# Performance work log

Measured on AMD Instinct MI355X. Metric: run time of the kernel, lower is better.

The kernel has to match this reference:

```python
import jax, jax.numpy as jnp
import numpy as np

MC = 16384
IND_T = 96
N_MAT = 4
N_STRIKES = 21


def _init_linear(key, fan_in, fan_out, prefix=()):
    k1, k2 = jax.random.split(key)
    lim = 1.0 / np.sqrt(fan_in)
    W = jax.random.uniform(k1, prefix + (fan_in, fan_out), minval=-lim, maxval=lim, dtype=jnp.float32)
    b = jax.random.uniform(k2, prefix + (fan_out,), minval=-lim, maxval=lim, dtype=jnp.float32)
    return W, b


def setup_inputs() -> dict:
    key = jax.random.key(0)
    ks = jax.random.split(key, 14)
    z = jax.random.normal(ks[0], (MC, IND_T), dtype=jnp.float32)
    zz = jax.random.normal(ks[1], (MC, IND_T), dtype=jnp.float32)
    timegrid = jnp.arange(IND_T + 1, dtype=jnp.float32) / 365.0  # daily grid
    maturities = jnp.array([24, 48, 72, 96], dtype=jnp.int32)    # in days
    strikes = jnp.linspace(0.8, 1.2, N_STRIKES, dtype=jnp.float32)
    sv_W1, sv_b1 = _init_linear(ks[2], 3, 100)
    sv_W2, sv_b2 = _init_linear(ks[3], 100, 100)
    sv_W3, sv_b3 = _init_linear(ks[4], 100, 1)
    vh_W1, vh_b1 = _init_linear(ks[5], 2, 20, (N_MAT,))
    vh_W2, vh_b2 = _init_linear(ks[6], 20, N_STRIKES, (N_MAT,))
    vd_W1, vd_b1 = _init_linear(ks[7], 1, 20)
    vd_W2, vd_b2 = _init_linear(ks[8], 20, 1)
    vv_W1, vv_b1 = _init_linear(ks[9], 1, 20)
    vv_W2, vv_b2 = _init_linear(ks[10], 20, 1)
    v0 = jax.random.uniform(ks[11], (1,), dtype=jnp.float32) * 0.1
    rho = jnp.ones((1,), dtype=jnp.float32) * -2.0
    return dict(S0=jnp.float32(1.0), rate=jnp.float32(0.05), z=z, zz=zz,
                timegrid=timegrid, strikes=strikes, v0=v0, rho=rho,
                sv_W1=sv_W1, sv_b1=sv_b1, sv_W2=sv_W2, sv_b2=sv_b2, sv_W3=sv_W3, sv_b3=sv_b3,
                vh_W1=vh_W1, vh_b1=vh_b1, vh_W2=vh_W2, vh_b2=vh_b2,
                vd_W1=vd_W1, vd_b1=vd_b1, vd_W2=vd_W2, vd_b2=vd_b2,
                vv_W1=vv_W1, vv_b1=vv_b1, vv_W2=vv_W2, vv_b2=vv_b2,
                maturities=maturities)


def reference(S0, rate, z, zz, timegrid, strikes, v0, rho,
              sv_W1, sv_b1, sv_W2, sv_b2, sv_W3, sv_b3,
              vh_W1, vh_b1, vh_W2, vh_b2,
              vd_W1, vd_b1, vd_W2, vd_b2,
              vv_W1, vv_b1, vv_W2, vv_b2,
              maturities):
    sg = jax.lax.stop_gradient
    mc = z.shape[0]
    n_mat = vh_W1.shape[0]
    n_strikes = strikes.shape[0]

    def s_vol(x):  # [MC,3] -> [MC,1], softplus output
        h1 = jax.nn.relu(x @ sv_W1 + sv_b1)
        h2 = jax.nn.relu(h1 @ sv_W2 + sv_b2)
        return jax.nn.softplus(h2 @ sv_W3 + sv_b3)

    def v_drift(v):  # [MC,1] -> [MC,1]
        return jax.nn.relu(v @ vd_W1 + vd_b1) @ vd_W2 + vd_b2

    def v_vol(v):  # [MC,1] -> [MC,1], softplus output
        return jax.nn.softplus(jax.nn.relu(v @ vv_W1 + vv_b1) @ vv_W2 + vv_b2)

    def vanilla_hedge_all(x):  # [MC,2] -> [MC, n_strikes, n_mat] (one net per maturity)
        h1 = jax.nn.relu(jnp.einsum('mi,kio->kmo', x, vh_W1) + vh_b1[:, None, :])
        out = jax.nn.softplus(jnp.einsum('kmo,koj->kmj', h1, vh_W2) + vh_b2[:, None, :])
        return jnp.transpose(out, (1, 2, 0))

    rho_t = jnp.tanh(rho)[0]
    days = jnp.round(timegrid * 365.0).astype(jnp.int32)       # [IND_T+1]
    le = days[1:, None] <= maturities[None, :]                  # [IND_T, n_mat]
    idx_net = jnp.argmax(le, axis=1)                            # first live maturity per step
    is_mat = jnp.any(days[1:, None] == maturities[None, :], axis=1)
    mat_idx = jnp.arange(n_mat)

    Slog0 = jnp.log(jnp.full((mc, 1), S0, dtype=jnp.float32))
    V0 = jnp.full((mc, 1), 1.0, dtype=jnp.float32) * jax.nn.sigmoid(v0)[0] * 0.5
    cv0 = jnp.zeros((mc, n_strikes, n_mat), dtype=jnp.float32)
    pv0 = jnp.zeros((n_mat, n_strikes), dtype=jnp.float32)

    xs = (z.T[:, :, None], zz.T[:, :, None], timegrid[:-1], timegrid[1:], idx_net, is_mat)

    def step(carry, x):
        Slog_old, V_old, cv, pv_h, pv_var = carry
        z_i, zz_i, t0, t1, idx, im = x
        h = t1 - t0
        sqh = jnp.sqrt(h)
        dW = sqh * z_i                                          # [MC,1]
        dB = rho_t * dW + jnp.sqrt(1.0 - rho_t ** 2) * sqh * zz_i
        ones_t = jnp.full((mc, 1), 1.0, dtype=jnp.float32) * t0
        pd = s_vol(jnp.concatenate([ones_t, Slog_old, V_old], axis=1))  # price diffusion
        cv_fwd = vanilla_hedge_all(jnp.concatenate([ones_t, sg(Slog_old)], axis=1))
        V_new = V_old + v_drift(V_old) * h + v_vol(V_old) * dB
        drift = rate - 0.5 * pd ** 2
        diff = pd * dW
        drift_c = 1.0 + jnp.abs(sg(drift)) * sqh                # tamed Euler
        diff_c = 1.0 + jnp.abs(sg(pd)) * sqh
        Slog_new = Slog_old + drift * h / drift_c + diff / diff_c
        S_new = jnp.exp(Slog_new)
        S_old = jnp.exp(Slog_old)
        dS = jnp.exp(-rate * t1) * S_new - jnp.exp(-rate * t0) * S_old  # [MC,1]
        mask = (mat_idx >= idx).astype(cv.dtype)                # live maturities only
        cv = cv + mask[None, None, :] * cv_fwd * sg(dS)[:, :, None]
        # hedged vanilla (call) prices collected at maturity steps
        payoff = jnp.exp(-rate * t1) * jnp.maximum(S_new - strikes[None, :], 0.0)
        price = payoff - cv[:, :, idx]                          # [MC, n_strikes]
        pv = jnp.mean(price, axis=0)
        pvar = jnp.var(price, axis=0, ddof=1)
        sel = (mat_idx == idx)[:, None] & im
        pv_h = jnp.where(sel, pv[None, :], pv_h)
        pv_var = jnp.where(sel, pvar[None, :], pv_var)
        return (Slog_new, V_new, cv, pv_h, pv_var), None

    (_, _, _, pv_h, pv_var), _ = jax.lax.scan(step, (Slog0, V0, cv0, pv0, pv0), xs)
    return jnp.stack([pv_h, pv_var])  # [2, n_mat, n_strikes]
```

## Files before the change

kernel.cpp:

```cpp
#include <hip/hip_runtime.h>
#include <hip/hip_bf16.h>
#include <math.h>


#define MC      16384
#define NSTEP   96
#define BLOCK   512
#define NGROUP  512
#define NPAIR   84

typedef short bf16x8 __attribute__((ext_vector_type(8)));
typedef float f32x4  __attribute__((ext_vector_type(4)));

union U8 { uint4 u; bf16x8 v; };
union BF2U { __hip_bfloat162 b; unsigned u; };

__device__ __forceinline__ unsigned bf16rne(float x) {
    unsigned u = __float_as_uint(x);
    return (u + 0x7FFFu + ((u >> 16) & 1u)) >> 16;
}
__device__ __forceinline__ unsigned pk2(float lo, float hi) {
    BF2U t; t.b = __float22bfloat162_rn(make_float2(lo, hi));
    return t.u;
}
__device__ __forceinline__ float sp(float x) {
    return fmaxf(x, 0.f) + __logf(1.f + __expf(-fabsf(x)));
}

__global__ __launch_bounds__(BLOCK, 4)
void lsv_sim(const float* __restrict__ S0p,   const float* __restrict__ ratep,
             const float* __restrict__ z,     const float* __restrict__ zzg,
             const float* __restrict__ strikesg,
             const float* __restrict__ v0p,   const float* __restrict__ rhop,
             const float* __restrict__ svW1,  const float* __restrict__ svb1,
             const float* __restrict__ svW2,  const float* __restrict__ svb2,
             const float* __restrict__ svW3,  const float* __restrict__ svb3,
             const float* __restrict__ vhW1,  const float* __restrict__ vhb1,
             const float* __restrict__ vhW2,  const float* __restrict__ vhb2,
             const float* __restrict__ vdW1,  const float* __restrict__ vdb1,
             const float* __restrict__ vdW2,  const float* __restrict__ vdb2,
             const float* __restrict__ vvW1,  const float* __restrict__ vvb1,
             const float* __restrict__ vvW2,  const float* __restrict__ vvb2,
             const int*   __restrict__ mats,
             float* __restrict__ psum, float* __restrict__ psq)
{
    __shared__ __align__(16) unsigned short H1c[16 * 32 * 8];
    __shared__ __align__(16) float W1f[16 * 32];
    __shared__ __align__(16) float WH1f[16 * 32];
    __shared__ __align__(16) float B2T[128], W3T[128];
    __shared__ __align__(16) float RED[32 * 4];
    __shared__ float VDb[2][32], VVb[2][32];
    __shared__ float PSs[2][32], PSq[2][32];
    __shared__ __align__(16) float VW[128];
    __shared__ __align__(16) float4 STEP[NSTEP];
    __shared__ float D1T[NSTEP];
    __shared__ int   ITAB[NSTEP];
    __shared__ float ZT[32][97], ZZT[32][97];
    __shared__ float SLOG[32], VST[32], SST[32], SLOGP[32], DSP[32];
    __shared__ __align__(16) float CW1[2][128];
    __shared__ __align__(16) float CH[2][128];

    const int tid  = threadIdx.x;
    const int lane = tid & 63;
    const int w    = __builtin_amdgcn_readfirstlane(tid >> 6);
    const int quad = lane >> 4;
    const int col  = lane & 15;
    const int lp   = lane & 31;

    const int pt = w & 1;
    const int jg = w >> 1;
    const int hm = w >> 1;
    const int path = pt * 16 + col;
    const int kc   = jg * 4 + quad;

    {
        const size_t gbase = (size_t)blockIdx.x * 32 * NSTEP;
        for (int e = tid; e < 32 * NSTEP; e += BLOCK) {
            const int p = e / NSTEP, ii = e - p * NSTEP;
            ZT[p][ii]  = z  [gbase + e];
            ZZT[p][ii] = zzg[gbase + e];
        }
    }
    for (int e = tid; e < 128; e += BLOCK) {
        float v = 0.f;
        if      (e < 20)             v = vdW1[e];
        else if (e < 40)             v = vdb1[e - 20];
        else if (e < 60)             v = vdW2[e - 40];
        else if (e >= 64 && e < 84)  v = vvW1[e - 64];
        else if (e >= 84 && e < 104) v = vvb1[e - 84];
        else if (e >= 104 && e < 124)v = vvW2[e - 104];
        else if (e == 124)           v = vdb2[0];
        else if (e == 125)           v = vvb2[0];
        VW[e] = v;
        B2T[e] = (e < 100) ? svb2[e] : 0.f;
        W3T[e] = (e < 100) ? svW3[e] : 0.f;
    }
    for (int e = tid; e < 512; e += BLOCK) {
        const int kc2 = e >> 5, r5 = e & 31, grp = r5 >> 3, kk = kc2 * 8 + (r5 & 7);
        float v = 0.f;
        if (kk < 100) v = (grp == 0) ? svW1[kk] : (grp == 1) ? svW1[100 + kk]
                        : (grp == 2) ? svW1[200 + kk] : svb1[kk];
        W1f[e] = v;
    }
    for (int e = tid; e < 512; e += BLOCK) {
        const int hq = e >> 5, r5 = e & 31, grp = r5 >> 3;
        const int hmm = hq >> 2, qq = hq & 3;
        const int j = qq * 8 + (r5 & 7);
        float v = 0.f;
        if (j < 20 && grp < 3)
            v = (grp == 0) ? vhW1[hmm * 40 + j] : (grp == 1) ? vhW1[hmm * 40 + 20 + j]
                                                : vhb1[hmm * 20 + j];
        WH1f[e] = v;
    }

    const float rate  = ratep[0];
    const float S0    = S0p[0];
    const float rho_t = tanhf(rhop[0]);
    const float srho  = sqrtf(1.f - rho_t * rho_t);
    const float b3    = svb3[0];

    if (tid < NSTEP) {
        const int i = tid;
        const float t0 = (float)i       * (1.f / 365.f);
        const float t1 = (float)(i + 1) * (1.f / 365.f);
        const float h  = t1 - t0;
        STEP[i] = make_float4(t0, h, sqrtf(h), __expf(-rate * t0));
        D1T[i]  = __expf(-rate * t1);
        const int day = i + 1;
        const int m0 = mats[0], m1 = mats[1], m2 = mats[2], m3 = mats[3];
        const int idx = (day > m0) + (day > m1) + (day > m2);
        const int mi  = (idx == 0) ? m0 : (idx == 1) ? m1 : (idx == 2) ? m2 : m3;
        ITAB[i] = idx | ((day == mi) ? 256 : 0);
    }

    bf16x8 Af[4][2];
#pragma unroll
    for (int c = 0; c < 4; c++)
#pragma unroll
        for (int t = 0; t < 2; t++) {
            U8 tt;
#pragma unroll
            for (int e2 = 0; e2 < 4; e2++) {
                const int k0 = 32 * c + 8 * quad + 2 * e2;
                const int j  = (2 * jg + t) * 16 + col;
                const float v0 = (k0     < 100 && j < 100) ? svW2[k0 * 100 + j]       : 0.f;
                const float v1 = (k0 + 1 < 100 && j < 100) ? svW2[(k0 + 1) * 100 + j] : 0.f;
                (&tt.u.x)[e2] = bf16rne(v0) | (bf16rne(v1) << 16);
            }
            Af[c][t] = tt.v;
        }
    bf16x8 Ah[2];
#pragma unroll
    for (int st = 0; st < 2; st++) {
        U8 tt;
#pragma unroll
        for (int e2 = 0; e2 < 4; e2++) {
            const int j0 = 8 * quad + 2 * e2, j1 = j0 + 1;
            const int s  = (st == 0) ? col : (16 + (col & 3) * 4 + (col >> 2));
            const float v0 = (j0 < 20 && s < 21) ? vhW2[hm * 420 + j0 * 21 + s] : 0.f;
            const float v1 = (j1 < 20 && s < 21) ? vhW2[hm * 420 + j1 * 21 + s] : 0.f;
            (&tt.u.x)[e2] = bf16rne(v0) | (bf16rne(v1) << 16);
        }
        Ah[st] = tt.v;
    }
    f32x4 c0h, c1h;
    float K0a[4], K1a[2];
#pragma unroll
    for (int r = 0; r < 4; r++) {
        const int s0 = quad * 4 + r;
        c0h[r] = vhb2[hm * 21 + s0];
        K0a[r] = strikesg[s0];
        const int s1 = 16 + r * 4 + quad;
        c1h[r] = (s1 < 21) ? vhb2[hm * 21 + s1] : 0.f;
        if (r < 2) K1a[r] = (s1 < 21) ? strikesg[s1] : 1e30f;
    }

    float Slog = __logf(S0);
    float S    = __expf(Slog);
    float V    = (1.f / (1.f + __expf(-v0p[0]))) * 0.5f;
    f32x4 cv0 = {0.f, 0.f, 0.f, 0.f};
    float cv1[2] = {0.f, 0.f};

    __syncthreads();

    if (tid < 128) {
        const float t00 = STEP[0].x;
        const int kk = tid;
        CW1[0][kk] = fmaf(t00, W1f[(kk >> 3) * 32 + (kk & 7)],
                               W1f[(kk >> 3) * 32 + 24 + (kk & 7)]);
    } else if (tid < 256) {
        const float t00 = STEP[0].x;
        const int e = tid - 128;
        CH[0][e] = fmaf(t00, WH1f[(e >> 3) * 32 + (e & 7)],
                             WH1f[(e >> 3) * 32 + 16 + (e & 7)]);
    }
    if (tid < 32) {
        SLOG[tid] = Slog;
        SST[tid]  = S;
        VST[tid]  = V;
    }

    __syncthreads();

    const int j0e = (2 * jg) * 16 + quad * 4;
    const float4 b2a = *reinterpret_cast<const float4*>(B2T + j0e);
    const float4 w3a = *reinterpret_cast<const float4*>(W3T + j0e);
    const float4 b2b = *reinterpret_cast<const float4*>(B2T + j0e + 16);
    const float4 w3b = *reinterpret_cast<const float4*>(W3T + j0e + 16);
    const float4 wsA = *reinterpret_cast<const float4*>(WH1f + kc * 32 + 8);
    const float4 wsB = *reinterpret_cast<const float4*>(WH1f + kc * 32 + 12);
    const float4 w1B0 = *reinterpret_cast<const float4*>(W1f + kc * 32 + 8);
    const float4 w1B1 = *reinterpret_cast<const float4*>(W1f + kc * 32 + 12);
    const float4 w1C0 = *reinterpret_cast<const float4*>(W1f + kc * 32 + 16);
    const float4 w1C1 = *reinterpret_cast<const float4*>(W1f + kc * 32 + 20);

    auto hedge_step = [&](int ip) {
        const int iv   = ITAB[ip];
        const int idxp = iv & 0xff;
        if (hm >= idxp) {
            const int hb = ip & 1;
            const float slp = SLOGP[path];
            U8 b;
            {
                const float4 ch4 = *reinterpret_cast<const float4*>(&CH[hb][kc * 8]);
                (&b.u.x)[0] = pk2(fmaxf(ch4.x + slp * wsA.x, 0.f),
                                  fmaxf(ch4.y + slp * wsA.y, 0.f));
                (&b.u.x)[1] = pk2(fmaxf(ch4.z + slp * wsA.z, 0.f),
                                  fmaxf(ch4.w + slp * wsA.w, 0.f));
            }
            {
                const float4 ch4 = *reinterpret_cast<const float4*>(&CH[hb][kc * 8 + 4]);
                (&b.u.x)[2] = pk2(fmaxf(ch4.x + slp * wsB.x, 0.f),
                                  fmaxf(ch4.y + slp * wsB.y, 0.f));
                (&b.u.x)[3] = pk2(fmaxf(ch4.z + slp * wsB.z, 0.f),
                                  fmaxf(ch4.w + slp * wsB.w, 0.f));
            }
            const f32x4 D0 = __builtin_amdgcn_mfma_f32_16x16x32_bf16(Ah[0], b.v, c0h, 0, 0, 0);
            const f32x4 D1 = __builtin_amdgcn_mfma_f32_16x16x32_bf16(Ah[1], b.v, c1h, 0, 0, 0);
            const float dsP = DSP[path];
#pragma unroll
            for (int r = 0; r < 4; r++)
                cv0[r] += sp(D0[r]) * dsP;
#pragma unroll
            for (int r = 0; r < 2; r++)
                cv1[r] += sp(D1[r]) * dsP;
            if ((iv & 256) && hm == idxp) {
                const float Sp  = SST[path];
                const float d1p = D1T[ip];
                float p0[4], q0[4], p1[2], q1[2];
#pragma unroll
                for (int r = 0; r < 4; r++) {
                    p0[r] = d1p * fmaxf(Sp - K0a[r], 0.f) - cv0[r];
                    q0[r] = p0[r] * p0[r];
                }
#pragma unroll
                for (int r = 0; r < 2; r++) {
                    p1[r] = d1p * fmaxf(Sp - K1a[r], 0.f) - cv1[r];
                    q1[r] = p1[r] * p1[r];
                }
#pragma unroll
                for (int o = 1; o <= 8; o <<= 1) {
#pragma unroll
                    for (int r = 0; r < 4; r++) {
                        p0[r] += __shfl_xor(p0[r], o);
                        q0[r] += __shfl_xor(q0[r], o);
                    }
#pragma unroll
                    for (int r = 0; r < 2; r++) {
                        p1[r] += __shfl_xor(p1[r], o);
                        q1[r] += __shfl_xor(q1[r], o);
                    }
                }
                if (col == 0) {
#pragma unroll
                    for (int r = 0; r < 4; r++) {
                        const int s0 = quad * 4 + r;
                        PSs[pt][s0] = p0[r];  PSq[pt][s0] = q0[r];
                    }
#pragma unroll
                    for (int r = 0; r < 2; r++) {
                        const int s1 = 16 + r * 4 + quad;
                        if (s1 < 21) { PSs[pt][s1] = p1[r];  PSq[pt][s1] = q1[r]; }
                    }
                }
            }
        }
    };

    auto ps_reduce = [&](int ip) {
        if (w == 0) {
            const int iv = ITAB[ip];
            if (iv & 256) {
                const int s = lane & 31;
                if (s < 21) {
                    const float* src = (lane >= 32) ? &PSq[0][0] : &PSs[0][0];
                    const float acc = src[s] + src[32 + s];
                    float* dst = (lane >= 32) ? psq : psum;
                    dst[((iv & 0xff) * 21 + s) * NGROUP + blockIdx.x] = acc;
                }
            }
        }
    };

    for (int i = 0; i < NSTEP; i++) {
        const int buf = i & 1;

        {
            const float slp = SLOG[path];
            const float vp  = VST[path];
            uint4 o;
            {
                const float4 cw = *reinterpret_cast<const float4*>(&CW1[buf][kc * 8]);
                const float x0 = fmaxf(cw.x + slp * w1B0.x + vp * w1C0.x, 0.f);
                const float x1 = fmaxf(cw.y + slp * w1B0.y + vp * w1C0.y, 0.f);
                const float x2 = fmaxf(cw.z + slp * w1B0.z + vp * w1C0.z, 0.f);
                const float x3 = fmaxf(cw.w + slp * w1B0.w + vp * w1C0.w, 0.f);
                o.x = pk2(x0, x1);
                o.y = pk2(x2, x3);
            }
            {
                const float4 cw = *reinterpret_cast<const float4*>(&CW1[buf][kc * 8 + 4]);
                const float x0 = fmaxf(cw.x + slp * w1B1.x + vp * w1C1.x, 0.f);
                const float x1 = fmaxf(cw.y + slp * w1B1.y + vp * w1C1.y, 0.f);
                const float x2 = fmaxf(cw.z + slp * w1B1.z + vp * w1C1.z, 0.f);
                const float x3 = fmaxf(cw.w + slp * w1B1.w + vp * w1C1.w, 0.f);
                o.z = pk2(x0, x1);
                o.w = pk2(x2, x3);
            }
            *reinterpret_cast<uint4*>(H1c + (kc * 32 + path) * 8) = o;
        }
        if (i > 0) hedge_step(i - 1);
        if (w == 0) {
            const float Vp = VST[lp];
            const float* bw = VW + ((lane >= 32) ? 64 : 0);
            float a2 = 0.f;
#pragma unroll
            for (int q5 = 0; q5 < 5; q5++) {
                const float4 w1 = *reinterpret_cast<const float4*>(bw + 4 * q5);
                const float4 b1 = *reinterpret_cast<const float4*>(bw + 20 + 4 * q5);
                const float4 w2 = *reinterpret_cast<const float4*>(bw + 40 + 4 * q5);
                a2 += fmaxf(Vp * w1.x + b1.x, 0.f) * w2.x;
                a2 += fmaxf(Vp * w1.y + b1.y, 0.f) * w2.y;
                a2 += fmaxf(Vp * w1.z + b1.z, 0.f) * w2.z;
                a2 += fmaxf(Vp * w1.w + b1.w, 0.f) * w2.w;
            }
            if (lane < 32) VDb[buf][lp] = a2; else VVb[buf][lp] = a2;
        }
        __syncthreads();

        {
            f32x4 d0 = {0.f, 0.f, 0.f, 0.f};
            f32x4 d1 = {0.f, 0.f, 0.f, 0.f};
#pragma unroll
            for (int c = 0; c < 4; c++) {
                const bf16x8 b = *reinterpret_cast<const bf16x8*>(
                    H1c + ((quad + 4 * c) * 32 + path) * 8);
                d0 = __builtin_amdgcn_mfma_f32_16x16x32_bf16(Af[c][0], b, d0, 0, 0, 0);
                d1 = __builtin_amdgcn_mfma_f32_16x16x32_bf16(Af[c][1], b, d1, 0, 0, 0);
            }
            float acc = fmaxf(d0[0] + b2a.x, 0.f) * w3a.x
                      + fmaxf(d0[1] + b2a.y, 0.f) * w3a.y
                      + fmaxf(d0[2] + b2a.z, 0.f) * w3a.z
                      + fmaxf(d0[3] + b2a.w, 0.f) * w3a.w
                      + fmaxf(d1[0] + b2b.x, 0.f) * w3b.x
                      + fmaxf(d1[1] + b2b.y, 0.f) * w3b.y
                      + fmaxf(d1[2] + b2b.z, 0.f) * w3b.z
                      + fmaxf(d1[3] + b2b.w, 0.f) * w3b.w;
            acc += __shfl_xor(acc, 16);
            acc += __shfl_xor(acc, 32);
            if (quad == 0)
                RED[path * 4 + jg] = acc;
        }
        if (i > 0) ps_reduce(i - 1);
        __syncthreads();

        if (w == 1) {
            const float4 rr = *reinterpret_cast<const float4*>(RED + lp * 4);
            const float pout = (rr.x + rr.y) + (rr.z + rr.w);
            const float pd = sp(pout + b3);
            const float vdv = VDb[buf][lp] + VW[124];
            const float vvv = sp(VVb[buf][lp] + VW[125]);
            const float4 u  = STEP[i];
            const float sqh = u.z;
            const float zi  = ZT[lp][i];
            const float zzi = ZZT[lp][i];
            const float dW = sqh * zi;
            const float dB = rho_t * dW + srho * sqh * zzi;
            const float Vold = VST[lp];
            const float Sold = SST[lp];
            const float SlogO = SLOG[lp];
            const float Vn = Vold + vdv * u.y + vvv * dB;
            const float drift   = rate - 0.5f * pd * pd;
            const float diff    = pd * dW;
            const float drift_c = 1.f + fabsf(drift) * sqh;
            const float diff_c  = 1.f + fabsf(pd) * sqh;
            const float Sln = SlogO + __fdividef(drift * u.y, drift_c) + __fdividef(diff, diff_c);
            const float Sn  = __expf(Sln);
            const float dS  = D1T[i] * Sn - u.w * Sold;
            if (lane < 32) {
                SLOGP[lp] = SlogO;  DSP[lp] = dS;
                SLOG[lp]  = Sln;    SST[lp] = Sn;  VST[lp] = Vn;
            }
        } else if ((w == 2 || w == 3) && i + 1 < NSTEP) {
            const float t0n = STEP[i + 1].x;
            const int kk = (w - 2) * 64 + lane;
            CW1[buf ^ 1][kk] = fmaf(t0n, W1f[(kk >> 3) * 32 + (kk & 7)],
                                         W1f[(kk >> 3) * 32 + 24 + (kk & 7)]);
        } else if ((w == 4 || w == 5) && i + 1 < NSTEP) {
            const float t0n = STEP[i + 1].x;
            const int e = (w - 4) * 64 + lane;
            CH[buf ^ 1][e] = fmaf(t0n, WH1f[(e >> 3) * 32 + (e & 7)],
                                       WH1f[(e >> 3) * 32 + 16 + (e & 7)]);
        }
        __syncthreads();
    }

    hedge_step(NSTEP - 1);
    __syncthreads();
    ps_reduce(NSTEP - 1);
}

__global__ void lsv_finalize(const float* __restrict__ psum,
                             const float* __restrict__ psq,
                             float* __restrict__ out)
{
    const int t    = blockIdx.x;
    const int lane = threadIdx.x;
    float s = 0.f, q = 0.f;
    for (int b = lane; b < NGROUP; b += 64) {
        s += psum[t * NGROUP + b];
        q += psq [t * NGROUP + b];
    }
#pragma unroll
    for (int o = 1; o <= 32; o <<= 1) {
        s += __shfl_xor(s, o);
        q += __shfl_xor(q, o);
    }
    if (lane == 0) {
        const float mean = s * (1.0f / (float)MC);
        const float var  = (q - (float)MC * mean * mean) * (1.0f / (float)(MC - 1));
        out[t]         = mean;
        out[NPAIR + t] = var;
    }
}

extern "C" void kernel_launch(void* const* d_in, const int* in_sizes, int n_in,
                              void* d_out, int out_size, void* d_ws, size_t ws_size,
                              hipStream_t stream)
{
    const float* S0    = (const float*)d_in[0];
    const float* rate  = (const float*)d_in[1];
    const float* z     = (const float*)d_in[2];
    const float* zz    = (const float*)d_in[3];
    const float* strikes = (const float*)d_in[5];
    const float* v0    = (const float*)d_in[6];
    const float* rho   = (const float*)d_in[7];
    const float* svW1  = (const float*)d_in[8];
    const float* svb1  = (const float*)d_in[9];
    const float* svW2  = (const float*)d_in[10];
    const float* svb2  = (const float*)d_in[11];
    const float* svW3  = (const float*)d_in[12];
    const float* svb3  = (const float*)d_in[13];
    const float* vhW1  = (const float*)d_in[14];
    const float* vhb1  = (const float*)d_in[15];
    const float* vhW2  = (const float*)d_in[16];
    const float* vhb2  = (const float*)d_in[17];
    const float* vdW1  = (const float*)d_in[18];
    const float* vdb1  = (const float*)d_in[19];
    const float* vdW2  = (const float*)d_in[20];
    const float* vdb2  = (const float*)d_in[21];
    const float* vvW1  = (const float*)d_in[22];
    const float* vvb1  = (const float*)d_in[23];
    const float* vvW2  = (const float*)d_in[24];
    const float* vvb2  = (const float*)d_in[25];
    const int*   mats  = (const int*)d_in[26];

    float* psum = (float*)d_ws;
    float* psq  = psum + NPAIR * NGROUP;

    hipLaunchKernelGGL(lsv_sim, dim3(NGROUP), dim3(BLOCK), 0, stream,
                       S0, rate, z, zz, strikes, v0, rho,
                       svW1, svb1, svW2, svb2, svW3, svb3,
                       vhW1, vhb1, vhW2, vhb2,
                       vdW1, vdb1, vdW2, vdb2,
                       vvW1, vvb1, vvW2, vvb2,
                       mats, psum, psq);

    hipLaunchKernelGGL(lsv_finalize, dim3(NPAIR), dim3(64), 0, stream,
                       psum, psq, (float*)d_out);
}
```

Baseline: 440.9 us.

## Move loop-invariant weights from registers to LDS to raise occupancy

Raises the launch bound's minimum blocks per SM from 4 to 6. Hedge biases, strikes and first-layer weight slices that were held in registers for the whole loop are now staged in shared memory and reloaded inside each step where they are used. The aim is to lower VGPR pressure so more waves fit per CU and latency is hidden better. The cost is extra LDS reads every step, and spilling if the compiler cannot meet the tighter register budget.

```diff
diff --git a/kernel.cpp b/kernel.cpp
--- a/kernel.cpp
+++ b/kernel.cpp
@@ -27,7 +27,7 @@
     return fmaxf(x, 0.f) + __logf(1.f + __expf(-fabsf(x)));
 }
 
-__global__ __launch_bounds__(BLOCK, 4)
+__global__ __launch_bounds__(BLOCK, 6)
 void lsv_sim(const float* __restrict__ S0p,   const float* __restrict__ ratep,
              const float* __restrict__ z,     const float* __restrict__ zzg,
              const float* __restrict__ strikesg,
@@ -48,6 +48,8 @@
     __shared__ __align__(16) float W1f[16 * 32];
     __shared__ __align__(16) float WH1f[16 * 32];
     __shared__ __align__(16) float B2T[128], W3T[128];
+    __shared__ __align__(16) float BH0[64], BH1[64];
+    __shared__ __align__(16) float SK0[16], SK1[16];
     __shared__ __align__(16) float RED[32 * 4];
     __shared__ float VDb[2][32], VVb[2][32];
     __shared__ float PSs[2][32], PSq[2][32];
@@ -95,6 +97,16 @@
         B2T[e] = (e < 100) ? svb2[e] : 0.f;
         W3T[e] = (e < 100) ? svW3[e] : 0.f;
     }
+    for (int e = tid; e < 64; e += BLOCK) {
+        const int hmm = e >> 4, q = (e >> 2) & 3, r = e & 3;
+        BH0[e] = vhb2[hmm * 21 + q * 4 + r];
+        const int s1 = 16 + r * 4 + q;
+        BH1[e] = (s1 < 21) ? vhb2[hmm * 21 + s1] : 0.f;
+    }
+    if (tid < 16) {
+        SK0[tid] = strikesg[tid];
+        SK1[tid] = (16 + tid < 21) ? strikesg[16 + tid] : 1e30f;
+    }
     for (int e = tid; e < 512; e += BLOCK) {
         const int kc2 = e >> 5, r5 = e & 31, grp = r5 >> 3, kk = kc2 * 8 + (r5 & 7);
         float v = 0.f;
@@ -163,17 +175,6 @@
         }
         Ah[st] = tt.v;
     }
-    f32x4 c0h, c1h;
-    float K0a[4], K1a[2];
-#pragma unroll
-    for (int r = 0; r < 4; r++) {
-        const int s0 = quad * 4 + r;
-        c0h[r] = vhb2[hm * 21 + s0];
-        K0a[r] = strikesg[s0];
-        const int s1 = 16 + r * 4 + quad;
-        c1h[r] = (s1 < 21) ? vhb2[hm * 21 + s1] : 0.f;
-        if (r < 2) K1a[r] = (s1 < 21) ? strikesg[s1] : 1e30f;
-    }
 
     float Slog = __logf(S0);
     float S    = __expf(Slog);
@@ -203,16 +204,6 @@
     __syncthreads();
 
     const int j0e = (2 * jg) * 16 + quad * 4;
-    const float4 b2a = *reinterpret_cast<const float4*>(B2T + j0e);
-    const float4 w3a = *reinterpret_cast<const float4*>(W3T + j0e);
-    const float4 b2b = *reinterpret_cast<const float4*>(B2T + j0e + 16);
-    const float4 w3b = *reinterpret_cast<const float4*>(W3T + j0e + 16);
-    const float4 wsA = *reinterpret_cast<const float4*>(WH1f + kc * 32 + 8);
-    const float4 wsB = *reinterpret_cast<const float4*>(WH1f + kc * 32 + 12);
-    const float4 w1B0 = *reinterpret_cast<const float4*>(W1f + kc * 32 + 8);
-    const float4 w1B1 = *reinterpret_cast<const float4*>(W1f + kc * 32 + 12);
-    const float4 w1C0 = *reinterpret_cast<const float4*>(W1f + kc * 32 + 16);
-    const float4 w1C1 = *reinterpret_cast<const float4*>(W1f + kc * 32 + 20);
 
     auto hedge_step = [&](int ip) {
         const int iv   = ITAB[ip];
@@ -220,23 +211,30 @@
         if (hm >= idxp) {
             const int hb = ip & 1;
             const float slp = SLOGP[path];
+            const float* Wp = WH1f + (hm * 4 + quad) * 32;
+            const float4 wsA = *reinterpret_cast<const float4*>(Wp + 8);
+            const float4 wsB = *reinterpret_cast<const float4*>(Wp + 12);
             U8 b;
             {
-                const float4 ch4 = *reinterpret_cast<const float4*>(&CH[hb][kc * 8]);
+                const float4 ch4 = *reinterpret_cast<const float4*>(&CH[hb][(hm * 4 + quad) * 8]);
                 (&b.u.x)[0] = pk2(fmaxf(ch4.x + slp * wsA.x, 0.f),
                                   fmaxf(ch4.y + slp * wsA.y, 0.f));
                 (&b.u.x)[1] = pk2(fmaxf(ch4.z + slp * wsA.z, 0.f),
                                   fmaxf(ch4.w + slp * wsA.w, 0.f));
             }
             {
-                const float4 ch4 = *reinterpret_cast<const float4*>(&CH[hb][kc * 8 + 4]);
+                const float4 ch4 = *reinterpret_cast<const float4*>(&CH[hb][(hm * 4 + quad) * 8 + 4]);
                 (&b.u.x)[2] = pk2(fmaxf(ch4.x + slp * wsB.x, 0.f),
                                   fmaxf(ch4.y + slp * wsB.y, 0.f));
                 (&b.u.x)[3] = pk2(fmaxf(ch4.z + slp * wsB.z, 0.f),
                                   fmaxf(ch4.w + slp * wsB.w, 0.f));
             }
-            const f32x4 D0 = __builtin_amdgcn_mfma_f32_16x16x32_bf16(Ah[0], b.v, c0h, 0, 0, 0);
-            const f32x4 D1 = __builtin_amdgcn_mfma_f32_16x16x32_bf16(Ah[1], b.v, c1h, 0, 0, 0);
+            const float4 bh0 = *reinterpret_cast<const float4*>(BH0 + hm * 16 + quad * 4);
+            const float4 bh1 = *reinterpret_cast<const float4*>(BH1 + hm * 16 + quad * 4);
+            const f32x4 c0 = {bh0.x, bh0.y, bh0.z, bh0.w};
+            const f32x4 c1 = {bh1.x, bh1.y, bh1.z, bh1.w};
+            const f32x4 D0 = __builtin_amdgcn_mfma_f32_16x16x32_bf16(Ah[0], b.v, c0, 0, 0, 0);
+            const f32x4 D1 = __builtin_amdgcn_mfma_f32_16x16x32_bf16(Ah[1], b.v, c1, 0, 0, 0);
             const float dsP = DSP[path];
 #pragma unroll
             for (int r = 0; r < 4; r++)
@@ -247,15 +245,18 @@
             if ((iv & 256) && hm == idxp) {
                 const float Sp  = SST[path];
                 const float d1p = D1T[ip];
+                const float4 k0 = *reinterpret_cast<const float4*>(SK0 + quad * 4);
                 float p0[4], q0[4], p1[2], q1[2];
-#pragma unroll
-                for (int r = 0; r < 4; r++) {
-                    p0[r] = d1p * fmaxf(Sp - K0a[r], 0.f) - cv0[r];
-                    q0[r] = p0[r] * p0[r];
-                }
+                p0[0] = d1p * fmaxf(Sp - k0.x, 0.f) - cv0[0];
+                p0[1] = d1p * fmaxf(Sp - k0.y, 0.f) - cv0[1];
+                p0[2] = d1p * fmaxf(Sp - k0.z, 0.f) - cv0[2];
+                p0[3] = d1p * fmaxf(Sp - k0.w, 0.f) - cv0[3];
+#pragma unroll
+                for (int r = 0; r < 4; r++) q0[r] = p0[r] * p0[r];
 #pragma unroll
                 for (int r = 0; r < 2; r++) {
-                    p1[r] = d1p * fmaxf(Sp - K1a[r], 0.f) - cv1[r];
+                    const float K = SK1[r * 4 + quad];
+                    p1[r] = d1p * fmaxf(Sp - K, 0.f) - cv1[r];
                     q1[r] = p1[r] * p1[r];
                 }
 #pragma unroll
@@ -308,24 +309,19 @@
         {
             const float slp = SLOG[path];
             const float vp  = VST[path];
+            const float* Wp = W1f + kc * 32;
             uint4 o;
-            {
-                const float4 cw = *reinterpret_cast<const float4*>(&CW1[buf][kc * 8]);
-                const float x0 = fmaxf(cw.x + slp * w1B0.x + vp * w1C0.x, 0.f);
-                const float x1 = fmaxf(cw.y + slp * w1B0.y + vp * w1C0.y, 0.f);
-                const float x2 = fmaxf(cw.z + slp * w1B0.z + vp * w1C0.z, 0.f);
-                const float x3 = fmaxf(cw.w + slp * w1B0.w + vp * w1C0.w, 0.f);
-                o.x = pk2(x0, x1);
-                o.y = pk2(x2, x3);
-            }
-            {
-                const float4 cw = *reinterpret_cast<const float4*>(&CW1[buf][kc * 8 + 4]);
-                const float x0 = fmaxf(cw.x + slp * w1B1.x + vp * w1C1.x, 0.f);
-                const float x1 = fmaxf(cw.y + slp * w1B1.y + vp * w1C1.y, 0.f);
-                const float x2 = fmaxf(cw.z + slp * w1B1.z + vp * w1C1.z, 0.f);
-                const float x3 = fmaxf(cw.w + slp * w1B1.w + vp * w1C1.w, 0.f);
-                o.z = pk2(x0, x1);
-                o.w = pk2(x2, x3);
+#pragma unroll
+            for (int hh = 0; hh < 2; hh++) {
+                const float4 b4 = *reinterpret_cast<const float4*>(Wp + 8 + hh * 4);
+                const float4 c4 = *reinterpret_cast<const float4*>(Wp + 16 + hh * 4);
+                const float4 cw = *reinterpret_cast<const float4*>(&CW1[buf][kc * 8 + hh * 4]);
+                const float x0 = fmaxf(cw.x + slp * b4.x + vp * c4.x, 0.f);
+                const float x1 = fmaxf(cw.y + slp * b4.y + vp * c4.y, 0.f);
+                const float x2 = fmaxf(cw.z + slp * b4.z + vp * c4.z, 0.f);
+                const float x3 = fmaxf(cw.w + slp * b4.w + vp * c4.w, 0.f);
+                (&o.x)[2 * hh]     = pk2(x0, x1);
+                (&o.x)[2 * hh + 1] = pk2(x2, x3);
             }
             *reinterpret_cast<uint4*>(H1c + (kc * 32 + path) * 8) = o;
         }
@@ -358,6 +354,10 @@
                 d0 = __builtin_amdgcn_mfma_f32_16x16x32_bf16(Af[c][0], b, d0, 0, 0, 0);
                 d1 = __builtin_amdgcn_mfma_f32_16x16x32_bf16(Af[c][1], b, d1, 0, 0, 0);
             }
+            const float4 b2a = *reinterpret_cast<const float4*>(B2T + j0e);
+            const float4 w3a = *reinterpret_cast<const float4*>(W3T + j0e);
+            const float4 b2b = *reinterpret_cast<const float4*>(B2T + j0e + 16);
+            const float4 w3b = *reinterpret_cast<const float4*>(W3T + j0e + 16);
             float acc = fmaxf(d0[0] + b2a.x, 0.f) * w3a.x
                       + fmaxf(d0[1] + b2a.y, 0.f) * w3a.y
                       + fmaxf(d0[2] + b2a.z, 0.f) * w3a.z
```

New measurement: 611.8 us. 1.39x slower.
